# Performance work log

Measured on AMD Instinct MI355X. Metric: run time of the kernel, lower is better.

Reference implementation:

```python
import jax, jax.numpy as jnp
import numpy as np

RATIO = 0.5
TEMP = 0.1


def setup_inputs() -> dict:
    key = jax.random.key(0)
    k1, k2, k3 = jax.random.split(key, 3)
    B, D = 4096, 4096
    im = jax.random.normal(k1, (B, D), dtype=jnp.float32)
    s = jax.random.normal(k2, (2 * B, D), dtype=jnp.float32)
    sims_local = jax.random.normal(k3, (B, 2 * B), dtype=jnp.float32)
    return {"im": im, "s": s, "sims_local": sims_local}


def reference(im, s, sims_local):
    B = im.shape[0]
    # fused global + local similarity: [B, 2B]
    sim = RATIO * sims_local + (1.0 - RATIO) * (im @ s.T)
    diag = jnp.diagonal(sim[:, :B])  # positives, [B]
    # vectorized replacement of the python double loop: zero out second-half
    # columns that exceed the row's diagonal (diagonal lives in first half,
    # so updates never feed back into the comparison -> exact equivalence).
    second = jnp.where(sim[:, B:] > diag[:, None], 0.0, sim[:, B:])
    sim = jnp.concatenate([sim[:, :B], second], axis=1)

    # i2t: logits per row = [positive (diag), all other 2B-1 entries];
    # CE with label 0 == logsumexp(full row) - positive (permutation-invariant).
    logits_i2t = sim / TEMP
    loss_i2t = jnp.mean(jax.nn.logsumexp(logits_i2t, axis=1) - diag / TEMP)

    # t2i: transpose, keep first B rows -> first block transposed, [B, B]
    t = sim[:, :B].T
    logits_t2i = t / TEMP
    loss_t2i = jnp.mean(jax.nn.logsumexp(logits_t2i, axis=1) - jnp.diagonal(t) / TEMP)

    return loss_i2t + loss_t2i
```

## Files before the change

### kernel.cpp

```cpp
#include <hip/hip_runtime.h>
#include <hip/hip_bf16.h>

typedef __attribute__((ext_vector_type(8))) short short8;
typedef __attribute__((ext_vector_type(4))) float floatx4;

#define B_ROWS 4096
#define N_COLS 8192
#define K_DIM  4096
#define INV_T  10.0f

__device__ __forceinline__ unsigned pack2bf16(float a, float b) {
    unsigned lo = (__float_as_uint(a) + 0x8000u) >> 16;
    unsigned hi = (__float_as_uint(b) + 0x8000u) & 0xFFFF0000u;
    return lo | hi;
}

__device__ __forceinline__ void gload_lds16(const void* g, void* l) {
    __builtin_amdgcn_global_load_lds(
        (const __attribute__((address_space(1))) void*)g,
        (__attribute__((address_space(3))) void*)l,
        16, 0, 0);
}

__global__ __launch_bounds__(256) void convert_diag_kernel(
    const float* __restrict__ im, const float* __restrict__ s,
    const float* __restrict__ sims,
    unsigned short* __restrict__ im_b, unsigned short* __restrict__ s_b,
    float* __restrict__ diag)
{
    const int row = blockIdx.x;
    const float4* srow = (const float4*)(s + (size_t)row * K_DIM);
    uint4* sb = (uint4*)(s_b + (size_t)row * K_DIM);
    const bool has_im = row < B_ROWS;
    const float4* arow = (const float4*)(im + (size_t)row * K_DIM);
    uint4* ab = (uint4*)(im_b + (size_t)row * K_DIM);

    float sum = 0.f;
    for (int i = threadIdx.x; i < K_DIM / 8; i += 256) {
        float4 y0 = srow[2 * i], y1 = srow[2 * i + 1];
        sb[i] = make_uint4(pack2bf16(y0.x, y0.y), pack2bf16(y0.z, y0.w),
                           pack2bf16(y1.x, y1.y), pack2bf16(y1.z, y1.w));
        if (has_im) {
            float4 x0 = arow[2 * i], x1 = arow[2 * i + 1];
            ab[i] = make_uint4(pack2bf16(x0.x, x0.y), pack2bf16(x0.z, x0.w),
                               pack2bf16(x1.x, x1.y), pack2bf16(x1.z, x1.w));
            sum += x0.x * y0.x + x0.y * y0.y + x0.z * y0.z + x0.w * y0.w;
            sum += x1.x * y1.x + x1.y * y1.y + x1.z * y1.z + x1.w * y1.w;
        }
    }
    if (has_im) {
        #pragma unroll
        for (int off = 1; off < 64; off <<= 1) sum += __shfl_xor(sum, off, 64);
        __shared__ float wsum[4];
        const int lane = threadIdx.x & 63, wid = threadIdx.x >> 6;
        if (lane == 0) wsum[wid] = sum;
        __syncthreads();
        if (threadIdx.x == 0) {
            float tot = wsum[0] + wsum[1] + wsum[2] + wsum[3];
            diag[row] = 0.5f * sims[(size_t)row * N_COLS + row] + 0.5f * tot;
        }
    }
}

__global__ __launch_bounds__(256) void gemm_loss_bf16_kernel(
    const unsigned short* __restrict__ im_b, const unsigned short* __restrict__ s_b,
    const float* __restrict__ sims, const float* __restrict__ diag,
    float* __restrict__ pi2t_m, float* __restrict__ pi2t_l,
    float* __restrict__ pt2i_m, float* __restrict__ pt2i_l)
{
    const int jt = blockIdx.x;
    const int it = blockIdx.y;
    const int tid = threadIdx.x;
    const int wid = tid >> 6, lane = tid & 63;
    const int wr = wid >> 1, wc = wid & 1;
    const int q = lane >> 4, cl = lane & 15;

    __shared__ __align__(16) unsigned short Asm[128 * 32];
    __shared__ __align__(16) unsigned short Bsm[128 * 32];
    __shared__ float sm_m[2][128], sm_l[2][128];
    __shared__ float sc_m[2][128], sc_l[2][128];

    const int r0 = (wid * 2 + 0) * 16 + (lane >> 2);
    const int r1 = (wid * 2 + 1) * 16 + (lane >> 2);
    const int kg = (lane & 3) * 8;
    const unsigned short* gA0 = im_b + (size_t)(it * 128 + r0) * K_DIM + kg;
    const unsigned short* gA1 = im_b + (size_t)(it * 128 + r1) * K_DIM + kg;
    const unsigned short* gB0 = s_b + (size_t)(jt * 128 + r0) * K_DIM + kg;
    const unsigned short* gB1 = s_b + (size_t)(jt * 128 + r1) * K_DIM + kg;
    unsigned short* lA0 = &Asm[(wid * 2 + 0) * 512];
    unsigned short* lA1 = &Asm[(wid * 2 + 1) * 512];
    unsigned short* lB0 = &Bsm[(wid * 2 + 0) * 512];
    unsigned short* lB1 = &Bsm[(wid * 2 + 1) * 512];

    floatx4 acc[4][4];
    #pragma unroll
    for (int i = 0; i < 4; ++i)
        #pragma unroll
        for (int j = 0; j < 4; ++j) acc[i][j] = (floatx4){0.f, 0.f, 0.f, 0.f};

    for (int kt = 0; kt < 128; ++kt) {
        gload_lds16(gA0, lA0);
        gload_lds16(gA1, lA1);
        gload_lds16(gB0, lB0);
        gload_lds16(gB1, lB1);
        gA0 += 32; gA1 += 32; gB0 += 32; gB1 += 32;
        __syncthreads();
        short8 av[4], bv[4];
        #pragma unroll
        for (int ty = 0; ty < 4; ++ty)
            av[ty] = *(const short8*)&Asm[(wr * 64 + ty * 16 + cl) * 32 + q * 8];
        #pragma unroll
        for (int tx = 0; tx < 4; ++tx)
            bv[tx] = *(const short8*)&Bsm[(wc * 64 + tx * 16 + cl) * 32 + q * 8];
        #pragma unroll
        for (int ty = 0; ty < 4; ++ty)
            #pragma unroll
            for (int tx = 0; tx < 4; ++tx)
                acc[ty][tx] = __builtin_amdgcn_mfma_f32_16x16x32_bf16(av[ty], bv[tx], acc[ty][tx], 0, 0, 0);
        __syncthreads();
    }

    const int row_base = it * 128 + wr * 64;
    const int col_base = jt * 128 + wc * 64;
    const bool second_half = (jt >= 32);

    float dv[4][4];
    #pragma unroll
    for (int ty = 0; ty < 4; ++ty)
        #pragma unroll
        for (int r = 0; r < 4; ++r)
            dv[ty][r] = diag[row_base + ty * 16 + q * 4 + r];

    #pragma unroll
    for (int ty = 0; ty < 4; ++ty) {
        #pragma unroll
        for (int tx = 0; tx < 4; ++tx) {
            const int col = col_base + tx * 16 + cl;
            #pragma unroll
            for (int r = 0; r < 4; ++r) {
                const int row = row_base + ty * 16 + q * 4 + r;
                float v = 0.5f * sims[(size_t)row * N_COLS + col] + 0.5f * acc[ty][tx][r];
                if (second_half && v > dv[ty][r]) v = 0.f;
                acc[ty][tx][r] = v * INV_T;
            }
        }
    }

    #pragma unroll
    for (int ty = 0; ty < 4; ++ty) {
        #pragma unroll
        for (int r = 0; r < 4; ++r) {
            float mx = fmaxf(fmaxf(acc[ty][0][r], acc[ty][1][r]),
                             fmaxf(acc[ty][2][r], acc[ty][3][r]));
            #pragma unroll
            for (int off = 1; off < 16; off <<= 1) mx = fmaxf(mx, __shfl_xor(mx, off, 64));
            float sum = 0.f;
            #pragma unroll
            for (int tx = 0; tx < 4; ++tx) sum += __expf(acc[ty][tx][r] - mx);
            #pragma unroll
            for (int off = 1; off < 16; off <<= 1) sum += __shfl_xor(sum, off, 64);
            if (cl == 0) {
                sm_m[wc][wr * 64 + ty * 16 + q * 4 + r] = mx;
                sm_l[wc][wr * 64 + ty * 16 + q * 4 + r] = sum;
            }
        }
    }

    if (!second_half) {
        #pragma unroll
        for (int tx = 0; tx < 4; ++tx) {
            float mx = -3.4e38f;
            #pragma unroll
            for (int ty = 0; ty < 4; ++ty)
                #pragma unroll
                for (int r = 0; r < 4; ++r) mx = fmaxf(mx, acc[ty][tx][r]);
            mx = fmaxf(mx, __shfl_xor(mx, 16, 64));
            mx = fmaxf(mx, __shfl_xor(mx, 32, 64));
            float sum = 0.f;
            #pragma unroll
            for (int ty = 0; ty < 4; ++ty)
                #pragma unroll
                for (int r = 0; r < 4; ++r) sum += __expf(acc[ty][tx][r] - mx);
            sum += __shfl_xor(sum, 16, 64);
            sum += __shfl_xor(sum, 32, 64);
            if (q == 0) {
                sc_m[wr][wc * 64 + tx * 16 + cl] = mx;
                sc_l[wr][wc * 64 + tx * 16 + cl] = sum;
            }
        }
    }

    __syncthreads();

    if (tid < 128) {
        float m0 = sm_m[0][tid], m1 = sm_m[1][tid];
        float mm = fmaxf(m0, m1);
        float ll = sm_l[0][tid] * __expf(m0 - mm) + sm_l[1][tid] * __expf(m1 - mm);
        pi2t_m[(size_t)jt * B_ROWS + it * 128 + tid] = mm;
        pi2t_l[(size_t)jt * B_ROWS + it * 128 + tid] = ll;
    } else if (!second_half) {
        const int t2 = tid - 128;
        float m0 = sc_m[0][t2], m1 = sc_m[1][t2];
        float mm = fmaxf(m0, m1);
        float ll = sc_l[0][t2] * __expf(m0 - mm) + sc_l[1][t2] * __expf(m1 - mm);
        pt2i_m[(size_t)it * B_ROWS + jt * 128 + t2] = mm;
        pt2i_l[(size_t)it * B_ROWS + jt * 128 + t2] = ll;
    }
}

__global__ __launch_bounds__(256) void diag_kernel(
    const float* __restrict__ im, const float* __restrict__ s,
    const float* __restrict__ sims, float* __restrict__ diag)
{
    const int row = blockIdx.x;
    const float4* a = (const float4*)(im + (size_t)row * K_DIM);
    const float4* b = (const float4*)(s  + (size_t)row * K_DIM);
    float sum = 0.f;
    for (int i = threadIdx.x; i < K_DIM / 4; i += 256) {
        float4 x = a[i], y = b[i];
        sum += x.x * y.x + x.y * y.y + x.z * y.z + x.w * y.w;
    }
    #pragma unroll
    for (int off = 1; off < 64; off <<= 1) sum += __shfl_xor(sum, off, 64);
    __shared__ float wsum[4];
    const int lane = threadIdx.x & 63, wid = threadIdx.x >> 6;
    if (lane == 0) wsum[wid] = sum;
    __syncthreads();
    if (threadIdx.x == 0) {
        float tot = wsum[0] + wsum[1] + wsum[2] + wsum[3];
        diag[row] = 0.5f * sims[(size_t)row * N_COLS + row] + 0.5f * tot;
    }
}

__global__ __launch_bounds__(256) void gemm_loss_kernel(
    const float* __restrict__ im, const float* __restrict__ s,
    const float* __restrict__ sims, const float* __restrict__ diag,
    float* __restrict__ pi2t_m, float* __restrict__ pi2t_l,
    float* __restrict__ pt2i_m, float* __restrict__ pt2i_l)
{
    const int jt = blockIdx.x;
    const int it = blockIdx.y;
    const int tid = threadIdx.x;
    const int wid = tid >> 6, lane = tid & 63;
    const int wr = wid >> 1, wc = wid & 1;
    const int q = lane >> 4, cl = lane & 15;

    __shared__ __align__(16) unsigned short Asm[128 * 32];
    __shared__ __align__(16) unsigned short Bsm[128 * 32];
    __shared__ float sm_m[2][128], sm_l[2][128];
    __shared__ float sc_m[2][128], sc_l[2][128];

    const int g0 = tid, g1 = tid + 256;
    const int r0 = g0 >> 2, c0 = (g0 & 3) * 8;
    const int r1 = g1 >> 2, c1 = (g1 & 3) * 8;
    const float* a0 = im + (size_t)(it * 128 + r0) * K_DIM + c0;
    const float* a1 = im + (size_t)(it * 128 + r1) * K_DIM + c1;
    const float* b0 = s  + (size_t)(jt * 128 + r0) * K_DIM + c0;
    const float* b1 = s  + (size_t)(jt * 128 + r1) * K_DIM + c1;
    const int la0 = r0 * 32 + c0, la1 = r1 * 32 + c1;

    floatx4 acc[4][4];
    #pragma unroll
    for (int i = 0; i < 4; ++i)
        #pragma unroll
        for (int j = 0; j < 4; ++j) acc[i][j] = (floatx4){0.f, 0.f, 0.f, 0.f};

    for (int kt = 0; kt < 128; ++kt) {
        float4 xa0 = *(const float4*)a0;
        float4 xa1 = *(const float4*)(a0 + 4);
        float4 ya0 = *(const float4*)a1;
        float4 ya1 = *(const float4*)(a1 + 4);
        float4 xb0 = *(const float4*)b0;
        float4 xb1 = *(const float4*)(b0 + 4);
        float4 yb0 = *(const float4*)b1;
        float4 yb1 = *(const float4*)(b1 + 4);
        a0 += 32; a1 += 32; b0 += 32; b1 += 32;
        __syncthreads();
        *(uint4*)&Asm[la0] = make_uint4(pack2bf16(xa0.x, xa0.y), pack2bf16(xa0.z, xa0.w),
                                        pack2bf16(xa1.x, xa1.y), pack2bf16(xa1.z, xa1.w));
        *(uint4*)&Asm[la1] = make_uint4(pack2bf16(ya0.x, ya0.y), pack2bf16(ya0.z, ya0.w),
                                        pack2bf16(ya1.x, ya1.y), pack2bf16(ya1.z, ya1.w));
        *(uint4*)&Bsm[la0] = make_uint4(pack2bf16(xb0.x, xb0.y), pack2bf16(xb0.z, xb0.w),
                                        pack2bf16(xb1.x, xb1.y), pack2bf16(xb1.z, xb1.w));
        *(uint4*)&Bsm[la1] = make_uint4(pack2bf16(yb0.x, yb0.y), pack2bf16(yb0.z, yb0.w),
                                        pack2bf16(yb1.x, yb1.y), pack2bf16(yb1.z, yb1.w));
        __syncthreads();
        short8 av[4], bv[4];
        #pragma unroll
        for (int ty = 0; ty < 4; ++ty)
            av[ty] = *(const short8*)&Asm[(wr * 64 + ty * 16 + cl) * 32 + q * 8];
        #pragma unroll
        for (int tx = 0; tx < 4; ++tx)
            bv[tx] = *(const short8*)&Bsm[(wc * 64 + tx * 16 + cl) * 32 + q * 8];
        #pragma unroll
        for (int ty = 0; ty < 4; ++ty)
            #pragma unroll
            for (int tx = 0; tx < 4; ++tx)
                acc[ty][tx] = __builtin_amdgcn_mfma_f32_16x16x32_bf16(av[ty], bv[tx], acc[ty][tx], 0, 0, 0);
    }

    const int row_base = it * 128 + wr * 64;
    const int col_base = jt * 128 + wc * 64;
    const bool second_half = (jt >= 32);

    float dv[4][4];
    #pragma unroll
    for (int ty = 0; ty < 4; ++ty)
        #pragma unroll
        for (int r = 0; r < 4; ++r)
            dv[ty][r] = diag[row_base + ty * 16 + q * 4 + r];

    #pragma unroll
    for (int ty = 0; ty < 4; ++ty) {
        #pragma unroll
        for (int tx = 0; tx < 4; ++tx) {
            const int col = col_base + tx * 16 + cl;
            #pragma unroll
            for (int r = 0; r < 4; ++r) {
                const int row = row_base + ty * 16 + q * 4 + r;
                float v = 0.5f * sims[(size_t)row * N_COLS + col] + 0.5f * acc[ty][tx][r];
                if (second_half && v > dv[ty][r]) v = 0.f;
                acc[ty][tx][r] = v * INV_T;
            }
        }
    }

    #pragma unroll
    for (int ty = 0; ty < 4; ++ty) {
        #pragma unroll
        for (int r = 0; r < 4; ++r) {
            float mx = fmaxf(fmaxf(acc[ty][0][r], acc[ty][1][r]),
                             fmaxf(acc[ty][2][r], acc[ty][3][r]));
            #pragma unroll
            for (int off = 1; off < 16; off <<= 1) mx = fmaxf(mx, __shfl_xor(mx, off, 64));
            float sum = 0.f;
            #pragma unroll
            for (int tx = 0; tx < 4; ++tx) sum += __expf(acc[ty][tx][r] - mx);
            #pragma unroll
            for (int off = 1; off < 16; off <<= 1) sum += __shfl_xor(sum, off, 64);
            if (cl == 0) {
                sm_m[wc][wr * 64 + ty * 16 + q * 4 + r] = mx;
                sm_l[wc][wr * 64 + ty * 16 + q * 4 + r] = sum;
            }
        }
    }

    if (!second_half) {
        #pragma unroll
        for (int tx = 0; tx < 4; ++tx) {
            float mx = -3.4e38f;
            #pragma unroll
            for (int ty = 0; ty < 4; ++ty)
                #pragma unroll
                for (int r = 0; r < 4; ++r) mx = fmaxf(mx, acc[ty][tx][r]);
            mx = fmaxf(mx, __shfl_xor(mx, 16, 64));
            mx = fmaxf(mx, __shfl_xor(mx, 32, 64));
            float sum = 0.f;
            #pragma unroll
            for (int ty = 0; ty < 4; ++ty)
                #pragma unroll
                for (int r = 0; r < 4; ++r) sum += __expf(acc[ty][tx][r] - mx);
            sum += __shfl_xor(sum, 16, 64);
            sum += __shfl_xor(sum, 32, 64);
            if (q == 0) {
                sc_m[wr][wc * 64 + tx * 16 + cl] = mx;
                sc_l[wr][wc * 64 + tx * 16 + cl] = sum;
            }
        }
    }

    __syncthreads();

    if (tid < 128) {
        float m0 = sm_m[0][tid], m1 = sm_m[1][tid];
        float mm = fmaxf(m0, m1);
        float ll = sm_l[0][tid] * __expf(m0 - mm) + sm_l[1][tid] * __expf(m1 - mm);
        pi2t_m[(size_t)jt * B_ROWS + it * 128 + tid] = mm;
        pi2t_l[(size_t)jt * B_ROWS + it * 128 + tid] = ll;
    } else if (!second_half) {
        const int t2 = tid - 128;
        float m0 = sc_m[0][t2], m1 = sc_m[1][t2];
        float mm = fmaxf(m0, m1);
        float ll = sc_l[0][t2] * __expf(m0 - mm) + sc_l[1][t2] * __expf(m1 - mm);
        pt2i_m[(size_t)it * B_ROWS + jt * 128 + t2] = mm;
        pt2i_l[(size_t)it * B_ROWS + jt * 128 + t2] = ll;
    }
}

__global__ __launch_bounds__(256) void combine_kernel(
    const float* __restrict__ pi2t_m, const float* __restrict__ pi2t_l,
    const float* __restrict__ pt2i_m, const float* __restrict__ pt2i_l,
    const float* __restrict__ diag, float* __restrict__ accum)
{
    const int gid = blockIdx.x * 256 + threadIdx.x;
    float term;
    if (gid < B_ROWS) {
        const int row = gid;
        float m = pi2t_m[row], l = pi2t_l[row];
        for (int ct = 1; ct < 64; ++ct) {
            float m2 = pi2t_m[(size_t)ct * B_ROWS + row];
            float l2 = pi2t_l[(size_t)ct * B_ROWS + row];
            float nm = fmaxf(m, m2);
            l = l * __expf(m - nm) + l2 * __expf(m2 - nm);
            m = nm;
        }
        term = m + __logf(l) - diag[row] * INV_T;
    } else {
        const int col = gid - B_ROWS;
        float m = pt2i_m[col], l = pt2i_l[col];
        for (int rt = 1; rt < 32; ++rt) {
            float m2 = pt2i_m[(size_t)rt * B_ROWS + col];
            float l2 = pt2i_l[(size_t)rt * B_ROWS + col];
            float nm = fmaxf(m, m2);
            l = l * __expf(m - nm) + l2 * __expf(m2 - nm);
            m = nm;
        }
        term = m + __logf(l) - diag[col] * INV_T;
    }
    #pragma unroll
    for (int off = 1; off < 64; off <<= 1) term += __shfl_xor(term, off, 64);
    __shared__ float bsum[4];
    if ((threadIdx.x & 63) == 0) bsum[threadIdx.x >> 6] = term;
    __syncthreads();
    if (threadIdx.x == 0) atomicAdd(accum, bsum[0] + bsum[1] + bsum[2] + bsum[3]);
}

__global__ void finalize_kernel(const float* __restrict__ accum, float* __restrict__ out) {
    out[0] = accum[0] * (1.0f / 4096.0f);
}

extern "C" void kernel_launch(void* const* d_in, const int* in_sizes, int n_in,
                              void* d_out, int out_size, void* d_ws, size_t ws_size,
                              hipStream_t stream)
{
    const float* im   = (const float*)d_in[0];
    const float* s    = (const float*)d_in[1];
    const float* sims = (const float*)d_in[2];
    float* out = (float*)d_out;

    const size_t im_b_bytes = (size_t)B_ROWS * K_DIM * 2;
    const size_t s_b_bytes  = (size_t)N_COLS * K_DIM * 2;
    const size_t f32_bytes  = (4096 + 2 * 64 * 4096 + 2 * 32 * 4096 + 1) * sizeof(float);
    const size_t need = im_b_bytes + s_b_bytes + f32_bytes;

    if (ws_size >= need) {
        unsigned short* im_b = (unsigned short*)d_ws;
        unsigned short* s_b  = (unsigned short*)((char*)d_ws + im_b_bytes);
        float* fbase  = (float*)((char*)d_ws + im_b_bytes + s_b_bytes);
        float* diag   = fbase;
        float* pi2t_m = diag + 4096;
        float* pi2t_l = pi2t_m + 64 * 4096;
        float* pt2i_m = pi2t_l + 64 * 4096;
        float* pt2i_l = pt2i_m + 32 * 4096;
        float* accum  = pt2i_l + 32 * 4096;

        hipMemsetAsync(accum, 0, sizeof(float), stream);
        convert_diag_kernel<<<N_COLS, 256, 0, stream>>>(im, s, sims, im_b, s_b, diag);
        gemm_loss_bf16_kernel<<<dim3(64, 32), 256, 0, stream>>>(im_b, s_b, sims, diag,
                                                                pi2t_m, pi2t_l, pt2i_m, pt2i_l);
        combine_kernel<<<32, 256, 0, stream>>>(pi2t_m, pi2t_l, pt2i_m, pt2i_l, diag, accum);
        finalize_kernel<<<1, 1, 0, stream>>>(accum, out);
    } else {
        float* ws = (float*)d_ws;
        float* diag   = ws;
        float* pi2t_m = diag + 4096;
        float* pi2t_l = pi2t_m + 64 * 4096;
        float* pt2i_m = pi2t_l + 64 * 4096;
        float* pt2i_l = pt2i_m + 32 * 4096;
        float* accum  = pt2i_l + 32 * 4096;

        hipMemsetAsync(accum, 0, sizeof(float), stream);
        diag_kernel<<<4096, 256, 0, stream>>>(im, s, sims, diag);
        gemm_loss_kernel<<<dim3(64, 32), 256, 0, stream>>>(im, s, sims, diag,
                                                           pi2t_m, pi2t_l, pt2i_m, pt2i_l);
        combine_kernel<<<32, 256, 0, stream>>>(pi2t_m, pi2t_l, pt2i_m, pt2i_l, diag, accum);
        finalize_kernel<<<1, 1, 0, stream>>>(accum, out);
    }
}
```

Baseline: 710.4 us.

## Double-buffer LDS tiles with XOR swizzle and drop atomic reduction

The GEMM main loop now double-buffers the A/B LDS tiles, prefetching the next K-slice via global_load_lds right after a single barrier. This removes the second barrier per iteration and overlaps global loads with MFMA work. The global-to-LDS k-group offset is XOR-swizzled by row, with matching swizzled read offsets, to reduce LDS bank conflicts. Launch bounds now request 3 blocks per CU. The final reduction writes per-block partials and sums them in a 64-thread finalize kernel, replacing the memset plus atomicAdd. The cost is double the LDS tile space and possible register pressure from the occupancy hint.

```diff
diff --git a/kernel.cpp b/kernel.cpp
--- a/kernel.cpp
+++ b/kernel.cpp
@@ -62,7 +62,7 @@
     }
 }
 
-__global__ __launch_bounds__(256) void gemm_loss_bf16_kernel(
+__global__ __launch_bounds__(256, 3) void gemm_loss_bf16_kernel(
     const unsigned short* __restrict__ im_b, const unsigned short* __restrict__ s_b,
     const float* __restrict__ sims, const float* __restrict__ diag,
     float* __restrict__ pi2t_m, float* __restrict__ pi2t_l,
@@ -75,22 +75,28 @@
     const int wr = wid >> 1, wc = wid & 1;
     const int q = lane >> 4, cl = lane & 15;
 
-    __shared__ __align__(16) unsigned short Asm[128 * 32];
-    __shared__ __align__(16) unsigned short Bsm[128 * 32];
+    __shared__ __align__(16) unsigned short Asm[2][128 * 32];
+    __shared__ __align__(16) unsigned short Bsm[2][128 * 32];
     __shared__ float sm_m[2][128], sm_l[2][128];
     __shared__ float sc_m[2][128], sc_l[2][128];
 
     const int r0 = (wid * 2 + 0) * 16 + (lane >> 2);
     const int r1 = (wid * 2 + 1) * 16 + (lane >> 2);
-    const int kg = (lane & 3) * 8;
+    const int kg = (((lane & 3) ^ ((lane >> 3) & 3))) * 8;
     const unsigned short* gA0 = im_b + (size_t)(it * 128 + r0) * K_DIM + kg;
     const unsigned short* gA1 = im_b + (size_t)(it * 128 + r1) * K_DIM + kg;
     const unsigned short* gB0 = s_b + (size_t)(jt * 128 + r0) * K_DIM + kg;
     const unsigned short* gB1 = s_b + (size_t)(jt * 128 + r1) * K_DIM + kg;
-    unsigned short* lA0 = &Asm[(wid * 2 + 0) * 512];
-    unsigned short* lA1 = &Asm[(wid * 2 + 1) * 512];
-    unsigned short* lB0 = &Bsm[(wid * 2 + 0) * 512];
-    unsigned short* lB1 = &Bsm[(wid * 2 + 1) * 512];
+    const int lo0 = (wid * 2 + 0) * 512;
+    const int lo1 = (wid * 2 + 1) * 512;
+
+    const int swA = (q ^ ((cl >> 1) & 3)) * 8;
+    int roffA[4], roffB[4];
+    #pragma unroll
+    for (int t = 0; t < 4; ++t) {
+        roffA[t] = (wr * 64 + t * 16 + cl) * 32 + swA;
+        roffB[t] = (wc * 64 + t * 16 + cl) * 32 + swA;
+    }
 
     floatx4 acc[4][4];
     #pragma unroll
@@ -98,26 +104,35 @@
         #pragma unroll
         for (int j = 0; j < 4; ++j) acc[i][j] = (floatx4){0.f, 0.f, 0.f, 0.f};
 
+    gload_lds16(gA0, &Asm[0][lo0]);
+    gload_lds16(gA1, &Asm[0][lo1]);
+    gload_lds16(gB0, &Bsm[0][lo0]);
+    gload_lds16(gB1, &Bsm[0][lo1]);
+    gA0 += 32; gA1 += 32; gB0 += 32; gB1 += 32;
+
     for (int kt = 0; kt < 128; ++kt) {
-        gload_lds16(gA0, lA0);
-        gload_lds16(gA1, lA1);
-        gload_lds16(gB0, lB0);
-        gload_lds16(gB1, lB1);
-        gA0 += 32; gA1 += 32; gB0 += 32; gB1 += 32;
+        const int cur = kt & 1;
         __syncthreads();
+        if (kt < 127) {
+            const int nxt = cur ^ 1;
+            gload_lds16(gA0, &Asm[nxt][lo0]);
+            gload_lds16(gA1, &Asm[nxt][lo1]);
+            gload_lds16(gB0, &Bsm[nxt][lo0]);
+            gload_lds16(gB1, &Bsm[nxt][lo1]);
+            gA0 += 32; gA1 += 32; gB0 += 32; gB1 += 32;
+        }
         short8 av[4], bv[4];
         #pragma unroll
         for (int ty = 0; ty < 4; ++ty)
-            av[ty] = *(const short8*)&Asm[(wr * 64 + ty * 16 + cl) * 32 + q * 8];
+            av[ty] = *(const short8*)&Asm[cur][roffA[ty]];
         #pragma unroll
         for (int tx = 0; tx < 4; ++tx)
-            bv[tx] = *(const short8*)&Bsm[(wc * 64 + tx * 16 + cl) * 32 + q * 8];
+            bv[tx] = *(const short8*)&Bsm[cur][roffB[tx]];
         #pragma unroll
         for (int ty = 0; ty < 4; ++ty)
             #pragma unroll
             for (int tx = 0; tx < 4; ++tx)
                 acc[ty][tx] = __builtin_amdgcn_mfma_f32_16x16x32_bf16(av[ty], bv[tx], acc[ty][tx], 0, 0, 0);
-        __syncthreads();
     }
 
     const int row_base = it * 128 + wr * 64;
@@ -390,7 +405,7 @@
 __global__ __launch_bounds__(256) void combine_kernel(
     const float* __restrict__ pi2t_m, const float* __restrict__ pi2t_l,
     const float* __restrict__ pt2i_m, const float* __restrict__ pt2i_l,
-    const float* __restrict__ diag, float* __restrict__ accum)
+    const float* __restrict__ diag, float* __restrict__ pblk)
 {
     const int gid = blockIdx.x * 256 + threadIdx.x;
     float term;
@@ -422,11 +437,14 @@
     __shared__ float bsum[4];
     if ((threadIdx.x & 63) == 0) bsum[threadIdx.x >> 6] = term;
     __syncthreads();
-    if (threadIdx.x == 0) atomicAdd(accum, bsum[0] + bsum[1] + bsum[2] + bsum[3]);
-}
-
-__global__ void finalize_kernel(const float* __restrict__ accum, float* __restrict__ out) {
-    out[0] = accum[0] * (1.0f / 4096.0f);
+    if (threadIdx.x == 0) pblk[blockIdx.x] = bsum[0] + bsum[1] + bsum[2] + bsum[3];
+}
+
+__global__ void finalize_kernel(const float* __restrict__ pblk, float* __restrict__ out) {
+    float v = (threadIdx.x < 32) ? pblk[threadIdx.x] : 0.f;
+    #pragma unroll
+    for (int off = 1; off < 64; off <<= 1) v += __shfl_xor(v, off, 64);
+    if (threadIdx.x == 0) out[0] = v * (1.0f / 4096.0f);
 }
 
 extern "C" void kernel_launch(void* const* d_in, const int* in_sizes, int n_in,
@@ -440,7 +458,7 @@
 
     const size_t im_b_bytes = (size_t)B_ROWS * K_DIM * 2;
     const size_t s_b_bytes  = (size_t)N_COLS * K_DIM * 2;
-    const size_t f32_bytes  = (4096 + 2 * 64 * 4096 + 2 * 32 * 4096 + 1) * sizeof(float);
+    const size_t f32_bytes  = (4096 + 2 * 64 * 4096 + 2 * 32 * 4096 + 32) * sizeof(float);
     const size_t need = im_b_bytes + s_b_bytes + f32_bytes;
 
     if (ws_size >= need) {
@@ -452,14 +470,13 @@
         float* pi2t_l = pi2t_m + 64 * 4096;
         float* pt2i_m = pi2t_l + 64 * 4096;
         float* pt2i_l = pt2i_m + 32 * 4096;
-        float* accum  = pt2i_l + 32 * 4096;
-
-        hipMemsetAsync(accum, 0, sizeof(float), stream);
+        float* pblk   = pt2i_l + 32 * 4096;
+
         convert_diag_kernel<<<N_COLS, 256, 0, stream>>>(im, s, sims, im_b, s_b, diag);
         gemm_loss_bf16_kernel<<<dim3(64, 32), 256, 0, stream>>>(im_b, s_b, sims, diag,
                                                                 pi2t_m, pi2t_l, pt2i_m, pt2i_l);
-        combine_kernel<<<32, 256, 0, stream>>>(pi2t_m, pi2t_l, pt2i_m, pt2i_l, diag, accum);
-        finalize_kernel<<<1, 1, 0, stream>>>(accum, out);
+        combine_kernel<<<32, 256, 0, stream>>>(pi2t_m, pi2t_l, pt2i_m, pt2i_l, diag, pblk);
+        finalize_kernel<<<1, 64, 0, stream>>>(pblk, out);
     } else {
         float* ws = (float*)d_ws;
         float* diag   = ws;
@@ -467,13 +484,12 @@
         float* pi2t_l = pi2t_m + 64 * 4096;
         float* pt2i_m = pi2t_l + 64 * 4096;
         float* pt2i_l = pt2i_m + 32 * 4096;
-        float* accum  = pt2i_l + 32 * 4096;
-
-        hipMemsetAsync(accum, 0, sizeof(float), stream);
+        float* pblk   = pt2i_l + 32 * 4096;
+
         diag_kernel<<<4096, 256, 0, stream>>>(im, s, sims, diag);
         gemm_loss_kernel<<<dim3(64, 32), 256, 0, stream>>>(im, s, sims, diag,
                                                            pi2t_m, pi2t_l, pt2i_m, pt2i_l);
-        combine_kernel<<<32, 256, 0, stream>>>(pi2t_m, pi2t_l, pt2i_m, pt2i_l, diag, accum);
-        finalize_kernel<<<1, 1, 0, stream>>>(accum, out);
-    }
-}
+        combine_kernel<<<32, 256, 0, stream>>>(pi2t_m, pi2t_l, pt2i_m, pt2i_l, diag, pblk);
+        finalize_kernel<<<1, 64, 0, stream>>>(pblk, out);
+    }
+}
```

Measured after the change: 678.4 us. 1.05x faster.
